# Optimization experiments

Measured on AMD Instinct MI355X. Metric: run time of the kernel, lower is better.

The kernel has to match this reference:

```python
import jax, jax.numpy as jnp
import numpy as np


def _sample_level(tables, gx, gy, align_corners):
    # tables: [3, C, H, W]; gx, gy: [3, P] grid coords in [-1, 1]
    # emulates F.grid_sample(mode='bilinear', padding_mode='border')
    def one(tab, x, y):
        C, H, W = tab.shape
        if align_corners:
            ix = (x + 1.0) * 0.5 * (W - 1)
            iy = (y + 1.0) * 0.5 * (H - 1)
        else:
            ix = ((x + 1.0) * W - 1.0) * 0.5
            iy = ((y + 1.0) * H - 1.0) * 0.5
        ix = jnp.clip(ix, 0.0, W - 1.0)  # border padding
        iy = jnp.clip(iy, 0.0, H - 1.0)
        x0 = jnp.floor(ix)
        y0 = jnp.floor(iy)
        wx = ix - x0
        wy = iy - y0
        x0i = x0.astype(jnp.int32)
        y0i = y0.astype(jnp.int32)
        x1i = jnp.minimum(x0i + 1, W - 1)
        y1i = jnp.minimum(y0i + 1, H - 1)
        v00 = tab[:, y0i, x0i]  # [C, P]
        v01 = tab[:, y0i, x1i]
        v10 = tab[:, y1i, x0i]
        v11 = tab[:, y1i, x1i]
        top = v00 * (1.0 - wx) + v01 * wx
        bot = v10 * (1.0 - wx) + v11 * wx
        return (top * (1.0 - wy) + bot * wy).T  # [P, C]

    return jax.vmap(one, in_axes=(0, 0, 0))(tables, gx, gy)  # [3, P, C]


def _hexplane(xyz, t, bounds, sps, tps):
    lead = xyz.shape[:-1]
    xyz = xyz.reshape(-1, 3)
    t = t.reshape(-1, t.shape[-1])
    xyzn = (xyz - bounds[:, 0, :]) / (bounds[:, 1, :] - bounds[:, 0, :])
    x, y, z = xyzn[:, 0], xyzn[:, 1], xyzn[:, 2]
    # spatial planes: xy, xz, yz; grid[...,0]->W, grid[...,1]->H
    sgx = jnp.stack([x, x, y]) * 2.0 - 1.0  # [3, P]
    sgy = jnp.stack([y, z, z]) * 2.0 - 1.0
    tt = t[:, 0]
    # temporal planes: (t, x), (t, y), (t, z); t -> W (dim_time), coord -> H (res)
    tgx = jnp.stack([tt, tt, tt]) * 2.0 - 1.0
    tgy = jnp.stack([x, y, z]) * 2.0 - 1.0
    sfeat = jnp.concatenate([_sample_level(sp, sgx, sgy, False) for sp in sps], axis=-1)  # [3, P, C*L]
    tfeat = jnp.concatenate([_sample_level(tp, tgx, tgy, True) for tp in tps], axis=-1)   # [3, P, C*L]
    feat = jnp.concatenate([sfeat, tfeat], axis=0)  # [6, P, C*L]
    val = jnp.transpose(feat, (1, 0, 2)).reshape(feat.shape[1], -1)  # [P, 6*C*L]
    return val.reshape(*lead, val.shape[-1])


def setup_inputs() -> dict:
    key = jax.random.key(0)
    N = 1_000_000
    C = 8
    T = 100
    STD = 0.1
    resolutions = [16, 32, 64, 128]
    ks = jax.random.split(key, 2 + 2 * len(resolutions))
    xyz = jax.random.uniform(ks[0], (N, 3), dtype=jnp.float32)
    t = jax.random.uniform(ks[1], (N, 1), dtype=jnp.float32)
    bounds = jnp.stack([jnp.zeros((1, 3), jnp.float32), jnp.ones((1, 3), jnp.float32)], axis=1)  # [1, 2, 3]
    inp = {"xyz": xyz, "t": t, "bounds": bounds}
    for i, r in enumerate(resolutions):
        inp[f"sp{i}"] = jax.random.uniform(ks[2 + i], (3, C, r, r), jnp.float32, -STD, STD)
        inp[f"tp{i}"] = jax.random.uniform(ks[2 + len(resolutions) + i], (3, C, r, T), jnp.float32, -STD, STD)
    return inp


def reference(xyz, t, bounds, sp0, sp1, sp2, sp3, tp0, tp1, tp2, tp3):
    return _hexplane(xyz, t, bounds, (sp0, sp1, sp2, sp3), (tp0, tp1, tp2, tp3))
```

## Files before the change

kernel.cpp:

```cpp
#include <hip/hip_runtime.h>
#include <hip/hip_bf16.h>

typedef float f32x2 __attribute__((ext_vector_type(2)));
typedef float f32x4 __attribute__((ext_vector_type(4)));
typedef unsigned int u32;
typedef u32 u32x4 __attribute__((ext_vector_type(4)));

#define Y_SP0 0
#define Y_SP1 13056
#define Y_SP2 63744
#define Y_TP0 263424
#define Y_TP1 340992
#define Y_TP2 496128
#define Y_TP3 806400
#define P_SP3 1426944

__global__ __launch_bounds__(256) void build_tabs(
    const float* __restrict__ sp0, const float* __restrict__ sp1,
    const float* __restrict__ sp2, const float* __restrict__ sp3,
    const float* __restrict__ tp0, const float* __restrict__ tp1,
    const float* __restrict__ tp2, const float* __restrict__ tp3,
    unsigned short* __restrict__ dst)
{
    int id = blockIdx.y;
    const float* src; int W, H, off; bool yp;
    switch (id) {
        case 0: src = sp0; W = 16;  H = 16;  off = Y_SP0; yp = true;  break;
        case 1: src = sp1; W = 32;  H = 32;  off = Y_SP1; yp = true;  break;
        case 2: src = sp2; W = 64;  H = 64;  off = Y_SP2; yp = true;  break;
        case 3: src = tp0; W = 100; H = 16;  off = Y_TP0; yp = true;  break;
        case 4: src = tp1; W = 100; H = 32;  off = Y_TP1; yp = true;  break;
        case 5: src = tp2; W = 100; H = 64;  off = Y_TP2; yp = true;  break;
        case 6: src = tp3; W = 100; H = 128; off = Y_TP3; yp = true;  break;
        default:src = sp3; W = 128; H = 128; off = P_SP3; yp = false; break;
    }
    int HW = W * H;
    int i = blockIdx.x * 256 + threadIdx.x;
    float v;
    if (yp) {
        int Wp = W + 1;
        int total = 3 * H * Wp * 16;
        if (i >= total) return;
        int half = i & 1;
        int c    = (i >> 1) & 7;
        int q    = i >> 4;
        int x  = q % Wp;
        int y  = (q / Wp) % H;
        int pl = q / (H * Wp);
        int xs = min(x, W - 1);
        int ys = half ? min(y + 1, H - 1) : y;
        v = src[(size_t)(pl * 8 + c) * HW + (size_t)ys * W + xs];
    } else {
        int total = 3 * HW * 8;
        if (i >= total) return;
        int c = i & 7;
        int q = i >> 3;
        int x  = q % W;
        int y  = (q / W) % H;
        int pl = q / HW;
        v = src[(size_t)(pl * 8 + c) * HW + (size_t)y * W + x];
    }
    __hip_bfloat16 b = __float2bfloat16(v);
    dst[off + i] = *reinterpret_cast<unsigned short*>(&b);
}

__device__ __forceinline__ float dot2bf(u32 ab, u32 w, float acc) {
    float d;
    asm("v_dot2_f32_bf16 %0, %1, %2, %3" : "=v"(d) : "v"(ab), "v"(w), "v"(acc));
    return d;
}
__device__ __forceinline__ u32 pk_bf16(float lo, float hi) {
    u32 d;
    asm("v_cvt_pk_bf16_f32 %0, %1, %2" : "=v"(d) : "v"(lo), "v"(hi));
    return d;
}

__global__ __launch_bounds__(192) void hexplane_yp(
    const float* __restrict__ xyz, const float* __restrict__ t,
    const float* __restrict__ bounds, const unsigned short* __restrict__ tw,
    float* __restrict__ out, int N)
{
    __shared__ float coords[8][4];
    __shared__ f32x4 lutA[24];
    __shared__ f32x4 lutB[24];
    __shared__ float ostage[1536];

    int tid = threadIdx.x;
    int n0  = blockIdx.x * 8;

    if (tid < 32) {
        int p = tid >> 2, comp = tid & 3;
        int n = n0 + p;
        float v = 0.0f;
        if (n < N) {
            if (comp < 3) {
                float b0 = bounds[comp], b1 = bounds[3 + comp];
                v = (xyz[(size_t)n * 3 + comp] - b0) / (b1 - b0);
            } else {
                v = t[n];
            }
        }
        coords[p][comp] = v;
    } else if (tid >= 64 && tid < 88) {
        int pos = tid - 64;
        int s = (pos < 9) ? pos + pos / 3 : (pos < 21) ? pos + 3 : 4 * (pos - 21) + 3;
        int g = s >> 2;
        int r = s & 3;
        int res = 16 << r;
        bool plain = (g < 3) && (r == 3);
        float sx, ox, sy, oy, cx, cy;
        int base_u, Ws, selx, sely;
        if (g < 3) {
            sx = (float)res; ox = -0.5f;
            sy = (float)res; oy = -0.5f;
            cx = (float)(res - 1); cy = (float)(res - 1);
            selx = (g == 2) ? 1 : 0;
            sely = (g == 0) ? 1 : 2;
            if (plain) {
                Ws = 128;
                base_u = P_SP3 + g * 128 * 128 * 8;
            } else {
                Ws = res + 1;
                int lo = (r == 0) ? Y_SP0 : (r == 1) ? Y_SP1 : Y_SP2;
                base_u = lo + g * res * (res + 1) * 16;
            }
        } else {
            int q = g - 3;
            Ws = 101;
            sx = 99.0f; ox = 0.0f;
            sy = (float)(res - 1); oy = 0.0f;
            cx = 99.0f; cy = (float)(res - 1);
            int lo = (r == 0) ? Y_TP0 : (r == 1) ? Y_TP1 : (r == 2) ? Y_TP2 : Y_TP3;
            base_u = lo + q * res * 101 * 16;
            selx = 3;
            sely = q;
        }
        int code = Ws | (selx << 9) | (sely << 12) | (plain ? (1 << 15) : 0) | (s << 16);
        f32x4 A = { sx, ox, sy, oy };
        f32x4 B = { cx, cy, __int_as_float(base_u * 2), __int_as_float(code) };
        lutA[pos] = A;
        lutB[pos] = B;
    }
    __syncthreads();

    int p   = tid & 7;
    int pos = tid >> 3;

    f32x4 A = lutA[pos];
    f32x4 B = lutB[pos];
    int code  = __float_as_int(B[3]);
    int Ws    = code & 511;
    int selx  = (code >> 9) & 7;
    int sely  = (code >> 12) & 7;
    bool plain = (code >> 15) & 1;
    int s     = (code >> 16) & 31;

    float fx = coords[p][selx];
    float fy = coords[p][sely];

    float ix = fmaf(fx, A[0], A[1]);
    float iy = fmaf(fy, A[2], A[3]);
    ix = fminf(fmaxf(ix, 0.0f), B[0]);
    iy = fminf(fmaxf(iy, 0.0f), B[1]);
    float x0f = floorf(ix), y0f = floorf(iy);
    float wx = ix - x0f, wy = iy - y0f;
    int x0 = (int)x0f, y0 = (int)y0f;
    float omx = 1.0f - wx, omy = 1.0f - wy;

    const char* tb = (const char*)tw + __float_as_int(B[2]);

    float f[8];
    if (!plain) {
        u32 wL = pk_bf16(omx * omy, omx * wy);
        u32 wR = pk_bf16(wx * omy,  wx * wy);
        const char* ad = tb + (size_t)(y0 * Ws + x0) * 32;
        u32x4 L0 = *(const u32x4*)(ad);
        u32x4 L1 = *(const u32x4*)(ad + 16);
        u32x4 L2 = *(const u32x4*)(ad + 32);
        u32x4 L3 = *(const u32x4*)(ad + 48);
        #pragma unroll
        for (int k = 0; k < 4; ++k) {
            f[k]     = dot2bf(L2[k], wR, dot2bf(L0[k], wL, 0.0f));
            f[4 + k] = dot2bf(L3[k], wR, dot2bf(L1[k], wL, 0.0f));
        }
    } else {
        u32 wT = pk_bf16(omx * omy, wx * omy);
        u32 wB = pk_bf16(omx * wy,  wx * wy);
        int x1 = min(x0 + 1, 127), y1 = min(y0 + 1, 127);
        u32x4 c00 = *(const u32x4*)(tb + (size_t)(y0 * 128 + x0) * 16);
        u32x4 c01 = *(const u32x4*)(tb + (size_t)(y0 * 128 + x1) * 16);
        u32x4 c10 = *(const u32x4*)(tb + (size_t)(y1 * 128 + x0) * 16);
        u32x4 c11 = *(const u32x4*)(tb + (size_t)(y1 * 128 + x1) * 16);
        #pragma unroll
        for (int k = 0; k < 4; ++k) {
            u32 tA = __builtin_amdgcn_perm(c00[k], c01[k], 0x01000504u);
            u32 tB = __builtin_amdgcn_perm(c00[k], c01[k], 0x03020706u);
            u32 bA = __builtin_amdgcn_perm(c10[k], c11[k], 0x01000504u);
            u32 bB = __builtin_amdgcn_perm(c10[k], c11[k], 0x03020706u);
            f[2*k]     = dot2bf(bA, wB, dot2bf(tA, wT, 0.0f));
            f[2*k + 1] = dot2bf(bB, wB, dot2bf(tB, wT, 0.0f));
        }
    }

    {
        int e = p * 24 + s;
        int q = p & 3;
        #pragma unroll
        for (int j = 0; j < 4; ++j) {
            f32x2 w2 = { f[2*j], f[2*j+1] };
            *(f32x2*)&ostage[e * 8 + (j ^ q) * 2] = w2;
        }
    }
    __syncthreads();

    size_t total_out = (size_t)N * 192;
    int a = tid & 1;

    int e0 = tid >> 1;
    int p0 = (e0 * 683) >> 14;
    int q0 = p0 & 3;
    int sg0 = a ^ (q0 >> 1);
    f32x4 v0 = *(f32x4*)&ostage[e0 * 8 + sg0 * 4];
    if (q0 & 1) { f32x4 tmp = { v0[2], v0[3], v0[0], v0[1] }; v0 = tmp; }

    int e1 = 96 + (tid >> 1);
    int p1 = (e1 * 683) >> 14;
    int q1 = p1 & 3;
    int sg1 = a ^ (q1 >> 1);
    f32x4 v1 = *(f32x4*)&ostage[e1 * 8 + sg1 * 4];
    if (q1 & 1) { f32x4 tmp = { v1[2], v1[3], v1[0], v1[1] }; v1 = tmp; }

    size_t F0 = (size_t)n0 * 192 + (size_t)tid * 4;
    size_t F1 = F0 + 768;
    if (F0 + 4 <= total_out)
        __builtin_nontemporal_store(v0, (f32x4*)(out + F0));
    if (F1 + 4 <= total_out)
        __builtin_nontemporal_store(v1, (f32x4*)(out + F1));
}

extern "C" void kernel_launch(void* const* d_in, const int* in_sizes, int n_in,
                              void* d_out, int out_size, void* d_ws, size_t ws_size,
                              hipStream_t stream) {
    const float* xyz    = (const float*)d_in[0];
    const float* t      = (const float*)d_in[1];
    const float* bounds = (const float*)d_in[2];
    const float* sp[4]  = { (const float*)d_in[3], (const float*)d_in[5],
                            (const float*)d_in[7], (const float*)d_in[9] };
    const float* tp[4]  = { (const float*)d_in[4], (const float*)d_in[6],
                            (const float*)d_in[8], (const float*)d_in[10] };
    float* out = (float*)d_out;

    int N = in_sizes[0] / 3;
    unsigned short* tw = (unsigned short*)d_ws;

    build_tabs<<<dim3(2424, 8), 256, 0, stream>>>(
        sp[0], sp[1], sp[2], sp[3], tp[0], tp[1], tp[2], tp[3], tw);

    int blocks = (N + 7) / 8;
    hexplane_yp<<<blocks, 192, 0, stream>>>(xyz, t, bounds, tw, out, N);
}
```

Before: 233.1 us.

## Process four point groups per block with software-pipelined gather prefetch

Each block now loops over four groups of eight points, reusing the per-block LUT setup and prefetching the next group's table loads while computing the current group's dot products. Coordinates are triple-buffered in shared memory and loaded two groups ahead. This is meant to hide gather latency and amortize setup, at the cost of fewer blocks and two barriers per group.

```diff
diff --git a/kernel.cpp b/kernel.cpp
--- a/kernel.cpp
+++ b/kernel.cpp
@@ -14,6 +14,8 @@
 #define Y_TP2 496128
 #define Y_TP3 806400
 #define P_SP3 1426944
+
+#define G 4
 
 __global__ __launch_bounds__(256) void build_tabs(
     const float* __restrict__ sp0, const float* __restrict__ sp1,
@@ -75,22 +77,22 @@
     return d;
 }
 
-__global__ __launch_bounds__(192) void hexplane_yp(
+__global__ __launch_bounds__(192) void hexplane_pipe(
     const float* __restrict__ xyz, const float* __restrict__ t,
     const float* __restrict__ bounds, const unsigned short* __restrict__ tw,
     float* __restrict__ out, int N)
 {
-    __shared__ float coords[8][4];
+    __shared__ float coords[3][8][4];
     __shared__ f32x4 lutA[24];
     __shared__ f32x4 lutB[24];
     __shared__ float ostage[1536];
 
-    int tid = threadIdx.x;
-    int n0  = blockIdx.x * 8;
-
-    if (tid < 32) {
-        int p = tid >> 2, comp = tid & 3;
-        int n = n0 + p;
+    int tid   = threadIdx.x;
+    int gbase = blockIdx.x * (G * 8);
+
+    if (tid < 64) {
+        int grp = tid >> 5, pp = (tid >> 2) & 7, comp = tid & 3;
+        int n = gbase + grp * 8 + pp;
         float v = 0.0f;
         if (n < N) {
             if (comp < 3) {
@@ -100,8 +102,8 @@
                 v = t[n];
             }
         }
-        coords[p][comp] = v;
-    } else if (tid >= 64 && tid < 88) {
+        coords[grp][pp][comp] = v;
+    } else if (tid < 88) {
         int pos = tid - 64;
         int s = (pos < 9) ? pos + pos / 3 : (pos < 21) ? pos + 3 : 4 * (pos - 21) + 3;
         int g = s >> 2;
@@ -154,88 +156,115 @@
     int sely  = (code >> 12) & 7;
     bool plain = (code >> 15) & 1;
     int s     = (code >> 16) & 31;
-
-    float fx = coords[p][selx];
-    float fy = coords[p][sely];
-
-    float ix = fmaf(fx, A[0], A[1]);
-    float iy = fmaf(fy, A[2], A[3]);
-    ix = fminf(fmaxf(ix, 0.0f), B[0]);
-    iy = fminf(fmaxf(iy, 0.0f), B[1]);
-    float x0f = floorf(ix), y0f = floorf(iy);
-    float wx = ix - x0f, wy = iy - y0f;
-    int x0 = (int)x0f, y0 = (int)y0f;
-    float omx = 1.0f - wx, omy = 1.0f - wy;
-
     const char* tb = (const char*)tw + __float_as_int(B[2]);
 
-    float f[8];
-    if (!plain) {
-        u32 wL = pk_bf16(omx * omy, omx * wy);
-        u32 wR = pk_bf16(wx * omy,  wx * wy);
-        const char* ad = tb + (size_t)(y0 * Ws + x0) * 32;
-        u32x4 L0 = *(const u32x4*)(ad);
-        u32x4 L1 = *(const u32x4*)(ad + 16);
-        u32x4 L2 = *(const u32x4*)(ad + 32);
-        u32x4 L3 = *(const u32x4*)(ad + 48);
-        #pragma unroll
-        for (int k = 0; k < 4; ++k) {
-            f[k]     = dot2bf(L2[k], wR, dot2bf(L0[k], wL, 0.0f));
-            f[4 + k] = dot2bf(L3[k], wR, dot2bf(L1[k], wL, 0.0f));
-        }
-    } else {
-        u32 wT = pk_bf16(omx * omy, wx * omy);
-        u32 wB = pk_bf16(omx * wy,  wx * wy);
-        int x1 = min(x0 + 1, 127), y1 = min(y0 + 1, 127);
-        u32x4 c00 = *(const u32x4*)(tb + (size_t)(y0 * 128 + x0) * 16);
-        u32x4 c01 = *(const u32x4*)(tb + (size_t)(y0 * 128 + x1) * 16);
-        u32x4 c10 = *(const u32x4*)(tb + (size_t)(y1 * 128 + x0) * 16);
-        u32x4 c11 = *(const u32x4*)(tb + (size_t)(y1 * 128 + x1) * 16);
-        #pragma unroll
-        for (int k = 0; k < 4; ++k) {
-            u32 tA = __builtin_amdgcn_perm(c00[k], c01[k], 0x01000504u);
-            u32 tB = __builtin_amdgcn_perm(c00[k], c01[k], 0x03020706u);
-            u32 bA = __builtin_amdgcn_perm(c10[k], c11[k], 0x01000504u);
-            u32 bB = __builtin_amdgcn_perm(c10[k], c11[k], 0x03020706u);
-            f[2*k]     = dot2bf(bA, wB, dot2bf(tA, wT, 0.0f));
-            f[2*k + 1] = dot2bf(bB, wB, dot2bf(tB, wT, 0.0f));
-        }
-    }
-
-    {
-        int e = p * 24 + s;
-        int q = p & 3;
-        #pragma unroll
-        for (int j = 0; j < 4; ++j) {
-            f32x2 w2 = { f[2*j], f[2*j+1] };
-            *(f32x2*)&ostage[e * 8 + (j ^ q) * 2] = w2;
-        }
-    }
-    __syncthreads();
+    int e   = p * 24 + s;
+    int k_w = p & 1;
+    float* bw0 = &ostage[e * 8 + (k_w ? 4 : 0)];
+    float* bw1 = &ostage[e * 8 + (k_w ? 0 : 4)];
+
+    int e0 = tid >> 1, a0 = tid & 1;
+    int p0 = (e0 * 683) >> 14;
+    const float* rd0 = &ostage[e0 * 8 + (a0 ^ (p0 & 1)) * 4];
+    int m1 = tid + 192;
+    int e1 = m1 >> 1, a1 = m1 & 1;
+    int p1 = (e1 * 683) >> 14;
+    const float* rd1 = &ostage[e1 * 8 + (a1 ^ (p1 & 1)) * 4];
+
+    u32 wA, wB_;
+    u32x4 L0, L1, L2, L3;
+
+    auto PREP = [&](int q) {
+        int cb = q % 3;
+        float fx = coords[cb][p][selx];
+        float fy = coords[cb][p][sely];
+        float ix = fmaf(fx, A[0], A[1]);
+        float iy = fmaf(fy, A[2], A[3]);
+        ix = fminf(fmaxf(ix, 0.0f), B[0]);
+        iy = fminf(fmaxf(iy, 0.0f), B[1]);
+        float x0f = floorf(ix), y0f = floorf(iy);
+        float wx = ix - x0f, wy = iy - y0f;
+        int x0 = (int)x0f, y0 = (int)y0f;
+        float omx = 1.0f - wx, omy = 1.0f - wy;
+        if (!plain) {
+            wA  = pk_bf16(omx * omy, omx * wy);
+            wB_ = pk_bf16(wx * omy,  wx * wy);
+            const char* ad = tb + (size_t)(y0 * Ws + x0) * 32;
+            L0 = *(const u32x4*)(ad);
+            L1 = *(const u32x4*)(ad + 16);
+            L2 = *(const u32x4*)(ad + 32);
+            L3 = *(const u32x4*)(ad + 48);
+        } else {
+            wA  = pk_bf16(omx * omy, wx * omy);
+            wB_ = pk_bf16(omx * wy,  wx * wy);
+            int x1 = min(x0 + 1, 127), y1 = min(y0 + 1, 127);
+            L0 = *(const u32x4*)(tb + (size_t)(y0 * 128 + x0) * 16);
+            L1 = *(const u32x4*)(tb + (size_t)(y0 * 128 + x1) * 16);
+            L2 = *(const u32x4*)(tb + (size_t)(y1 * 128 + x0) * 16);
+            L3 = *(const u32x4*)(tb + (size_t)(y1 * 128 + x1) * 16);
+        }
+    };
+
+    PREP(0);
 
     size_t total_out = (size_t)N * 192;
-    int a = tid & 1;
-
-    int e0 = tid >> 1;
-    int p0 = (e0 * 683) >> 14;
-    int q0 = p0 & 3;
-    int sg0 = a ^ (q0 >> 1);
-    f32x4 v0 = *(f32x4*)&ostage[e0 * 8 + sg0 * 4];
-    if (q0 & 1) { f32x4 tmp = { v0[2], v0[3], v0[0], v0[1] }; v0 = tmp; }
-
-    int e1 = 96 + (tid >> 1);
-    int p1 = (e1 * 683) >> 14;
-    int q1 = p1 & 3;
-    int sg1 = a ^ (q1 >> 1);
-    f32x4 v1 = *(f32x4*)&ostage[e1 * 8 + sg1 * 4];
-    if (q1 & 1) { f32x4 tmp = { v1[2], v1[3], v1[0], v1[1] }; v1 = tmp; }
-
-    size_t F0 = (size_t)n0 * 192 + (size_t)tid * 4;
-    size_t F1 = F0 + 768;
-    if (F0 + 4 <= total_out)
-        __builtin_nontemporal_store(v0, (f32x4*)(out + F0));
-    if (F1 + 4 <= total_out)
-        __builtin_nontemporal_store(v1, (f32x4*)(out + F1));
+    size_t outbase   = (size_t)blockIdx.x * (G * 1536);
+
+    for (int g = 0; g < G; ++g) {
+        float f[8];
+        if (!plain) {
+            #pragma unroll
+            for (int k = 0; k < 4; ++k) {
+                f[k]     = dot2bf(L2[k], wB_, dot2bf(L0[k], wA, 0.0f));
+                f[4 + k] = dot2bf(L3[k], wB_, dot2bf(L1[k], wA, 0.0f));
+            }
+        } else {
+            #pragma unroll
+            for (int k = 0; k < 4; ++k) {
+                u32 tA2 = __builtin_amdgcn_perm(L0[k], L1[k], 0x01000504u);
+                u32 tB2 = __builtin_amdgcn_perm(L0[k], L1[k], 0x03020706u);
+                u32 bA2 = __builtin_amdgcn_perm(L2[k], L3[k], 0x01000504u);
+                u32 bB2 = __builtin_amdgcn_perm(L2[k], L3[k], 0x03020706u);
+                f[2*k]     = dot2bf(bA2, wB_, dot2bf(tA2, wA, 0.0f));
+                f[2*k + 1] = dot2bf(bB2, wB_, dot2bf(tB2, wA, 0.0f));
+            }
+        }
+
+        if (g + 1 < G) PREP(g + 1);
+
+        *(f32x4*)bw0 = *(f32x4*)&f[0];
+        *(f32x4*)bw1 = *(f32x4*)&f[4];
+
+        float vc = 0.0f;
+        bool doc = (g + 2 < G) && (tid < 32);
+        if (doc) {
+            int comp = tid & 3;
+            int n = gbase + (g + 2) * 8 + (tid >> 2);
+            if (n < N) {
+                if (comp < 3) {
+                    float b0 = bounds[comp], b1 = bounds[3 + comp];
+                    vc = (xyz[(size_t)n * 3 + comp] - b0) / (b1 - b0);
+                } else {
+                    vc = t[n];
+                }
+            }
+        }
+
+        __syncthreads();
+
+        f32x4 v0 = *(const f32x4*)rd0;
+        f32x4 v1 = *(const f32x4*)rd1;
+        size_t F0 = outbase + (size_t)g * 1536 + (size_t)tid * 4;
+        size_t F1 = F0 + 768;
+        if (F0 + 4 <= total_out)
+            __builtin_nontemporal_store(v0, (f32x4*)(out + F0));
+        if (F1 + 4 <= total_out)
+            __builtin_nontemporal_store(v1, (f32x4*)(out + F1));
+
+        if (doc) coords[(g + 2) % 3][tid >> 2][tid & 3] = vc;
+
+        __syncthreads();
+    }
 }
 
 extern "C" void kernel_launch(void* const* d_in, const int* in_sizes, int n_in,
@@ -256,6 +285,6 @@
     build_tabs<<<dim3(2424, 8), 256, 0, stream>>>(
         sp[0], sp[1], sp[2], sp[3], tp[0], tp[1], tp[2], tp[3], tw);
 
-    int blocks = (N + 7) / 8;
-    hexplane_yp<<<blocks, 192, 0, stream>>>(xyz, t, bounds, tw, out, N);
-}
+    int blocks = (N + G * 8 - 1) / (G * 8);
+    hexplane_pipe<<<blocks, 192, 0, stream>>>(xyz, t, bounds, tw, out, N);
+}
```

New measurement: 222.9 us, median of 2. 4.4% less time.
